# Kernel optimization log

Hardware: AMD Instinct MI355X
Metric: run time of the kernel (lower is better)

The kernel has to match this reference:

```python
import jax, jax.numpy as jnp
import numpy as np

B, T, C, H = 2048, 64, 128, 8
HD = C // H  # head_size = 16
EPS = 1e-5


def layernorm(x, gamma, beta):
    mean = x.mean(-1, keepdims=True)
    var = ((x - mean) ** 2).mean(-1, keepdims=True)  # unbiased=False
    return gamma * (x - mean) / jnp.sqrt(var + EPS) + beta


def setup_inputs() -> dict:
    key = jax.random.key(0)
    ks = jax.random.split(key, 12)
    s_attn = 1.0 / np.sqrt(C)
    s_ff1 = 1.0 / np.sqrt(C)
    s_ff2 = 1.0 / np.sqrt(4 * C)
    return {
        "x": jax.random.normal(ks[0], (B, T, C), dtype=jnp.float32),
        # per-head q/k/v projections, stored (in,out) layout: [H, C, HD]
        "wq": jax.random.normal(ks[1], (H, C, HD), dtype=jnp.float32) * s_attn,
        "wk": jax.random.normal(ks[2], (H, C, HD), dtype=jnp.float32) * s_attn,
        "wv": jax.random.normal(ks[3], (H, C, HD), dtype=jnp.float32) * s_attn,
        "w_proj": jax.random.normal(ks[4], (C, C), dtype=jnp.float32) * s_attn,
        "b_proj": jnp.zeros((C,), dtype=jnp.float32),
        "w1": jax.random.normal(ks[5], (C, 4 * C), dtype=jnp.float32) * s_ff1,
        "b1": jnp.zeros((4 * C,), dtype=jnp.float32),
        "w2": jax.random.normal(ks[6], (4 * C, C), dtype=jnp.float32) * s_ff2,
        "b2": jnp.zeros((C,), dtype=jnp.float32),
        "g1": jnp.ones((C,), dtype=jnp.float32),
        "beta1": jnp.zeros((C,), dtype=jnp.float32),
        "g2": jnp.ones((C,), dtype=jnp.float32),
        "beta2": jnp.zeros((C,), dtype=jnp.float32),
    }


def reference(x, wq, wk, wv, w_proj, b_proj, w1, b1, w2, b2, g1, beta1, g2, beta2):
    # Dropout layers act as identity (eval mode).
    h = layernorm(x, g1, beta1)
    q = jnp.einsum("btc,hcd->bhtd", h, wq)
    k = jnp.einsum("btc,hcd->bhtd", h, wk)
    v = jnp.einsum("btc,hcd->bhtd", h, wv)
    wei = jnp.einsum("bhtd,bhsd->bhts", q, k) * (HD ** -0.5)
    Tcur = x.shape[1]
    causal = jnp.tril(jnp.ones((Tcur, Tcur), dtype=bool))
    wei = jnp.where(causal, wei, -jnp.inf)
    wei = jax.nn.softmax(wei, axis=-1)
    attn = jnp.einsum("bhts,bhsd->bhtd", wei, v)
    # concat heads in order along feature dim -> [B, T, C]
    attn = attn.transpose(0, 2, 1, 3).reshape(x.shape[0], Tcur, C)
    x = x + attn @ w_proj + b_proj
    h2 = layernorm(x, g2, beta2)
    ff = jax.nn.gelu(h2 @ w1 + b1, approximate=False) @ w2 + b2
    return x + ff
```

## Files before the change

kernel.cpp:

```cpp
#include <hip/hip_runtime.h>
#include <hip/hip_bf16.h>
#include <math.h>

#define CC  128
#define RLD 136
#define VLD 72

typedef __attribute__((ext_vector_type(8))) short bf16x8;
typedef __attribute__((ext_vector_type(4))) float f32x4;

#define MFMA16(a, b, c) __builtin_amdgcn_mfma_f32_16x16x32_bf16((a), (b), (c), 0, 0, 0)

__device__ __forceinline__ unsigned short f2bf(float f) {
    unsigned int u = __float_as_uint(f);
    u += 0x7FFFu + ((u >> 16) & 1u);
    return (unsigned short)(u >> 16);
}
__device__ __forceinline__ float bf2f(unsigned short h) {
    return __uint_as_float(((unsigned int)h) << 16);
}
__device__ __forceinline__ unsigned int f2bf2u(float lo, float hi) {
    __hip_bfloat162 h = __float22bfloat162_rn(make_float2(lo, hi));
    union { __hip_bfloat162 h2; unsigned int u; } cv; cv.h2 = h;
    return cv.u;
}
__device__ __forceinline__ bf16x8 mk_bf16x8(unsigned int a0, unsigned int a1,
                                            unsigned int a2, unsigned int a3) {
    union { uint4 u; bf16x8 b; } cv;
    cv.u = make_uint4(a0, a1, a2, a3);
    return cv.b;
}
__device__ __forceinline__ float gelu_tanh(float v) {
    float t = v * fmaf(0.102951871f, v * v, 2.302110084f);
    float s = __builtin_amdgcn_exp2f(t);
    return v - v * __builtin_amdgcn_rcpf(1.0f + s);
}

__global__ void pack_w(const float* __restrict__ src, unsigned short* __restrict__ dst,
                       int K, int N, int mode, float scale) {
    int i = blockIdx.x * 256 + threadIdx.x;
    if (i >= K * N) return;
    int j   = i & 7;
    int l   = (i >> 3) & 63;
    int tkt = i >> 9;
    int KT  = K >> 5;
    int nt  = tkt / KT;
    int kt  = tkt - nt * KT;
    int lg  = l >> 4;
    int k;
    if (mode == 2) {
        int kp = (j < 4) ? (lg * 4 + j) : (16 + lg * 4 + (j - 4));
        k = kt * 32 + kp;
    } else {
        k = kt * 32 + lg * 8 + j;
    }
    int n = nt * 16 + (l & 15);
    float v = (mode == 1) ? src[(n >> 4) * (K * 16) + k * 16 + (n & 15)]
                          : src[k * N + n];
    dst[i] = f2bf(v * scale);
}

#define OQ  0
#define OKk 16384
#define OV  32768
#define OP  49152
#define O1  65536
#define O2  131072

__global__ __launch_bounds__(512, 4) void block_fused(
    const float* __restrict__ x,
    const unsigned short* __restrict__ wpk,
    const float* __restrict__ bp,
    const float* __restrict__ b1, const float* __restrict__ b2,
    const float* __restrict__ g1, const float* __restrict__ be1,
    const float* __restrict__ g2, const float* __restrict__ be2,
    float* __restrict__ out)
{
    __shared__ __align__(16) unsigned short A [9216];
    __shared__ __align__(16) unsigned short Bq[8704];
    __shared__ __align__(16) unsigned short Ck[8704];
    __shared__ __align__(16) unsigned short Vv[9216];

    const int tid  = threadIdx.x;
    const int lane = tid & 63;
    const int wave = tid >> 6;
    const int l15  = lane & 15;
    const int lg   = lane >> 4;

    const float* xb = x   + (size_t)blockIdx.x * (64 * CC);
    float*       ob = out + (size_t)blockIdx.x * (64 * CC);

    {
        float ga = g1[lane], gb = g1[lane + 64], ba = be1[lane], bb = be1[lane + 64];
        for (int r = wave * 8; r < wave * 8 + 8; ++r) {
            float v0 = xb[r * CC + lane], v1 = xb[r * CC + lane + 64];
            float s = v0 + v1;
            float q = fmaf(v0, v0, v1 * v1);
            #pragma unroll
            for (int off = 32; off; off >>= 1) {
                s += __shfl_xor(s, off);
                q += __shfl_xor(q, off);
            }
            float mean = s * (1.0f / CC);
            float var  = fmaf(-mean, mean, q * (1.0f / CC));
            float rstd = __builtin_amdgcn_rsqf(var + 1e-5f);
            float d0 = v0 - mean, d1 = v1 - mean;
            unsigned int u = f2bf2u(fmaf(ga, d0 * rstd, ba), fmaf(gb, d1 * rstd, bb));
            A[r * RLD + lane]      = (unsigned short)u;
            A[r * RLD + lane + 64] = (unsigned short)(u >> 16);
        }
    }
    __syncthreads();

    const int rt  = wave >> 1;
    const int cg  = wave & 1;
    const int row0 = rt * 16 + lg * 4;
    const int hcol = wave * 16;

    {
        const unsigned short* wqb = wpk + OQ  + wave * 2048;
        const unsigned short* wkb = wpk + OKk + wave * 2048;
        const unsigned short* wvb = wpk + OV  + wave * 2048;
        bf16x8 wq4[4], wk4[4], wv4[4];
        #pragma unroll
        for (int kt = 0; kt < 4; ++kt) {
            wq4[kt] = *(const bf16x8*)&wqb[(kt * 64 + lane) * 8];
            wk4[kt] = *(const bf16x8*)&wkb[(kt * 64 + lane) * 8];
            wv4[kt] = *(const bf16x8*)&wvb[(kt * 64 + lane) * 8];
        }
        #pragma unroll
        for (int rt2 = 0; rt2 < 4; ++rt2) {
            bf16x8 la[4];
            #pragma unroll
            for (int kt = 0; kt < 4; ++kt)
                la[kt] = *(const bf16x8*)&A[(rt2 * 16 + l15) * RLD + kt * 32 + lg * 8];
            f32x4 cq = {0.f,0.f,0.f,0.f}, ck = {0.f,0.f,0.f,0.f}, cv = {0.f,0.f,0.f,0.f};
            #pragma unroll
            for (int kt = 0; kt < 4; ++kt) {
                cq = MFMA16(la[kt], wq4[kt], cq);
                ck = MFMA16(la[kt], wk4[kt], ck);
                cv = MFMA16(la[kt], wv4[kt], cv);
            }
            int rw = rt2 * 16 + lg * 4;
            unsigned int q01 = f2bf2u(cq[0], cq[1]), q23 = f2bf2u(cq[2], cq[3]);
            unsigned int k01 = f2bf2u(ck[0], ck[1]), k23 = f2bf2u(ck[2], ck[3]);
            unsigned int v01 = f2bf2u(cv[0], cv[1]), v23 = f2bf2u(cv[2], cv[3]);
            int o = rw * RLD + hcol + l15;
            Bq[o]           = (unsigned short)q01;
            Bq[o + RLD]     = (unsigned short)(q01 >> 16);
            Bq[o + 2 * RLD] = (unsigned short)q23;
            Bq[o + 3 * RLD] = (unsigned short)(q23 >> 16);
            Ck[o]           = (unsigned short)k01;
            Ck[o + RLD]     = (unsigned short)(k01 >> 16);
            Ck[o + 2 * RLD] = (unsigned short)k23;
            Ck[o + 3 * RLD] = (unsigned short)(k23 >> 16);
            int vslot = (rt2 >> 1) * 32 + lg * 8 + (rt2 & 1) * 4;
            *(uint2*)&Vv[(hcol + l15) * VLD + vslot] = make_uint2(v01, v23);
        }
    }

    float xpre[16];
    #pragma unroll
    for (int ntl = 0; ntl < 4; ++ntl) {
        int col = (cg * 4 + ntl) * 16 + l15;
        #pragma unroll
        for (int r = 0; r < 4; ++r)
            xpre[ntl * 4 + r] = xb[(row0 + r) * CC + col];
    }

    {
        bf16x8 zf = {0, 0, 0, 0, 0, 0, 0, 0};
        bf16x8 kf[4];
        #pragma unroll
        for (int st = 0; st < 4; ++st)
            kf[st] = (lane < 32) ? *(const bf16x8*)&Ck[(st * 16 + l15) * RLD + hcol + lg * 8] : zf;
        bf16x8 bvf[2];
        #pragma unroll
        for (int kt = 0; kt < 2; ++kt)
            bvf[kt] = *(const bf16x8*)&Vv[(hcol + l15) * VLD + kt * 32 + lg * 8];

        f32x4 ocs[4];
        #pragma unroll
        for (int mt = 0; mt < 4; ++mt) {
            bf16x8 qf = zf;
            if (lane < 32)
                qf = *(const bf16x8*)&Bq[(mt * 16 + l15) * RLD + hcol + lg * 8];
            f32x4 sfr[4];
            #pragma unroll
            for (int st = 0; st < 4; ++st) {
                sfr[st] = (f32x4){0.f, 0.f, 0.f, 0.f};
                if (st <= mt) sfr[st] = MFMA16(kf[st], qf, sfr[st]);
            }
            float e[4][4];
            float sum = 0.f;
            #pragma unroll
            for (int st = 0; st < 4; ++st) {
                #pragma unroll
                for (int r = 0; r < 4; ++r) {
                    float ev = 0.f;
                    if (st < mt) ev = __builtin_amdgcn_exp2f(sfr[st][r]);
                    else if (st == mt)
                        ev = (lg * 4 + r <= l15) ? __builtin_amdgcn_exp2f(sfr[st][r]) : 0.f;
                    e[st][r] = ev;
                    sum += ev;
                }
            }
            sum += __shfl_xor(sum, 16);
            sum += __shfl_xor(sum, 32);
            float inv = __builtin_amdgcn_rcpf(sum);
            unsigned int u[4][2];
            #pragma unroll
            for (int st = 0; st < 4; ++st) {
                if (st <= mt) {
                    u[st][0] = f2bf2u(e[st][0] * inv, e[st][1] * inv);
                    u[st][1] = f2bf2u(e[st][2] * inv, e[st][3] * inv);
                } else { u[st][0] = 0u; u[st][1] = 0u; }
            }
            f32x4 oc = {0.f, 0.f, 0.f, 0.f};
            #pragma unroll
            for (int kt = 0; kt < 2; ++kt) {
                if (kt <= (mt >> 1)) {
                    bf16x8 pa = mk_bf16x8(u[2 * kt][0], u[2 * kt][1],
                                          u[2 * kt + 1][0], u[2 * kt + 1][1]);
                    oc = MFMA16(pa, bvf[kt], oc);
                }
            }
            ocs[mt] = oc;
        }
        #pragma unroll
        for (int mt = 0; mt < 4; ++mt) {
            unsigned int u01 = f2bf2u(ocs[mt][0], ocs[mt][1]);
            unsigned int u23 = f2bf2u(ocs[mt][2], ocs[mt][3]);
            int o = (mt * 16 + lg * 4) * RLD + hcol + l15;
            Bq[o]           = (unsigned short)u01;
            Bq[o + RLD]     = (unsigned short)(u01 >> 16);
            Bq[o + 2 * RLD] = (unsigned short)u23;
            Bq[o + 3 * RLD] = (unsigned short)(u23 >> 16);
        }
    }
    __syncthreads();

    {
        bf16x8 pa[4];
        #pragma unroll
        for (int kt = 0; kt < 4; ++kt)
            pa[kt] = *(const bf16x8*)&Bq[(rt * 16 + l15) * RLD + kt * 32 + lg * 8];
        #pragma unroll
        for (int ntl = 0; ntl < 4; ++ntl) {
            int nt = cg * 4 + ntl;
            f32x4 c = {0.f, 0.f, 0.f, 0.f};
            #pragma unroll
            for (int kt = 0; kt < 4; ++kt) {
                bf16x8 b = *(const bf16x8*)&wpk[OP + ((nt * 4 + kt) * 64 + lane) * 8];
                c = MFMA16(pa[kt], b, c);
            }
            int col = nt * 16 + l15;
            float bpv = bp[col];
            unsigned int u01 = f2bf2u(xpre[ntl * 4 + 0] + c[0] + bpv,
                                      xpre[ntl * 4 + 1] + c[1] + bpv);
            unsigned int u23 = f2bf2u(xpre[ntl * 4 + 2] + c[2] + bpv,
                                      xpre[ntl * 4 + 3] + c[3] + bpv);
            int o = row0 * RLD + col;
            Ck[o]           = (unsigned short)u01;
            Ck[o + RLD]     = (unsigned short)(u01 >> 16);
            Ck[o + 2 * RLD] = (unsigned short)u23;
            Ck[o + 3 * RLD] = (unsigned short)(u23 >> 16);
        }
    }
    __syncthreads();

    {
        float ga = g2[lane], gb = g2[lane + 64], ba = be2[lane], bb = be2[lane + 64];
        for (int r = wave * 8; r < wave * 8 + 8; ++r) {
            float v0 = bf2f(Ck[r * RLD + lane]), v1 = bf2f(Ck[r * RLD + lane + 64]);
            float s = v0 + v1;
            float q = fmaf(v0, v0, v1 * v1);
            #pragma unroll
            for (int off = 32; off; off >>= 1) {
                s += __shfl_xor(s, off);
                q += __shfl_xor(q, off);
            }
            float mean = s * (1.0f / CC);
            float var  = fmaf(-mean, mean, q * (1.0f / CC));
            float rstd = __builtin_amdgcn_rsqf(var + 1e-5f);
            float d0 = v0 - mean, d1 = v1 - mean;
            unsigned int u = f2bf2u(fmaf(ga, d0 * rstd, ba), fmaf(gb, d1 * rstd, bb));
            A[r * RLD + lane]      = (unsigned short)u;
            A[r * RLD + lane + 64] = (unsigned short)(u >> 16);
        }
    }
    __syncthreads();

    {
        bf16x8 ha[4];
        #pragma unroll
        for (int kt = 0; kt < 4; ++kt)
            ha[kt] = *(const bf16x8*)&A[(rt * 16 + l15) * RLD + kt * 32 + lg * 8];
        f32x4 facc[8];
        #pragma unroll
        for (int n = 0; n < 8; ++n) facc[n] = (f32x4){0.f, 0.f, 0.f, 0.f};

        #pragma unroll 1
        for (int c = 0; c < 8; ++c) {
            int t0 = cg * 16 + 2 * c;
            f32x4 c0 = {0.f,0.f,0.f,0.f}, c1 = {0.f,0.f,0.f,0.f};
            #pragma unroll
            for (int kt = 0; kt < 4; ++kt) {
                bf16x8 w0 = *(const bf16x8*)&wpk[O1 + ((t0 * 4 + kt) * 64 + lane) * 8];
                bf16x8 w1f = *(const bf16x8*)&wpk[O1 + (((t0 + 1) * 4 + kt) * 64 + lane) * 8];
                c0 = MFMA16(w0,  ha[kt], c0);
                c1 = MFMA16(w1f, ha[kt], c1);
            }
            int fb = t0 * 16 + lg * 4;
            float g0[4], g1v[4];
            #pragma unroll
            for (int r = 0; r < 4; ++r) g0[r]  = gelu_tanh(c0[r] + b1[fb + r]);
            #pragma unroll
            for (int r = 0; r < 4; ++r) g1v[r] = gelu_tanh(c1[r] + b1[fb + 16 + r]);
            bf16x8 pa = mk_bf16x8(f2bf2u(g0[0],  g0[1]),  f2bf2u(g0[2],  g0[3]),
                                  f2bf2u(g1v[0], g1v[1]), f2bf2u(g1v[2], g1v[3]));
            int kc = cg * 8 + c;
            #pragma unroll
            for (int nt = 0; nt < 8; ++nt) {
                bf16x8 b = *(const bf16x8*)&wpk[O2 + ((nt * 16 + kc) * 64 + lane) * 8];
                facc[nt] = MFMA16(pa, b, facc[nt]);
            }
        }

        __syncthreads();
        float* fb0 = (rt < 2) ? (float*)A : (float*)Vv;
        const int fbase = (rt & 1) * 2112;
        if (cg == 0) {
            #pragma unroll
            for (int nt = 0; nt < 8; ++nt)
                #pragma unroll
                for (int r = 0; r < 4; ++r)
                    fb0[fbase + (lg * 4 + r) * 132 + nt * 16 + l15] = facc[nt][r];
        }
        __syncthreads();
        if (cg == 1) {
            #pragma unroll
            for (int nt = 0; nt < 8; ++nt) {
                int col = nt * 16 + l15;
                float b2v = b2[col];
                #pragma unroll
                for (int r = 0; r < 4; ++r) {
                    int row = row0 + r;
                    ob[row * CC + col] = bf2f(Ck[row * RLD + col]) + facc[nt][r]
                                       + fb0[fbase + (lg * 4 + r) * 132 + col] + b2v;
                }
            }
        }
    }
}

extern "C" void kernel_launch(void* const* d_in, const int* in_sizes, int n_in,
                              void* d_out, int out_size, void* d_ws, size_t ws_size,
                              hipStream_t stream) {
    (void)n_in; (void)out_size; (void)ws_size;
    const float* x   = (const float*)d_in[0];
    const float* wq  = (const float*)d_in[1];
    const float* wk  = (const float*)d_in[2];
    const float* wv  = (const float*)d_in[3];
    const float* wp  = (const float*)d_in[4];
    const float* bp  = (const float*)d_in[5];
    const float* w1  = (const float*)d_in[6];
    const float* b1  = (const float*)d_in[7];
    const float* w2  = (const float*)d_in[8];
    const float* b2  = (const float*)d_in[9];
    const float* g1  = (const float*)d_in[10];
    const float* be1 = (const float*)d_in[11];
    const float* g2  = (const float*)d_in[12];
    const float* be2 = (const float*)d_in[13];

    unsigned short* ws16 = (unsigned short*)d_ws;
    pack_w<<<64,  256, 0, stream>>>(wq, ws16 + OQ,  128, 128, 1, 0.3606737602f);
    pack_w<<<64,  256, 0, stream>>>(wk, ws16 + OKk, 128, 128, 1, 1.0f);
    pack_w<<<64,  256, 0, stream>>>(wv, ws16 + OV,  128, 128, 1, 1.0f);
    pack_w<<<64,  256, 0, stream>>>(wp, ws16 + OP,  128, 128, 0, 1.0f);
    pack_w<<<256, 256, 0, stream>>>(w1, ws16 + O1,  128, 512, 0, 1.0f);
    pack_w<<<256, 256, 0, stream>>>(w2, ws16 + O2,  512, 128, 2, 1.0f);

    int nblk = in_sizes[0] / (64 * CC);
    block_fused<<<dim3(nblk), dim3(512), 0, stream>>>(
        x, ws16, bp, b1, b2, g1, be1, g2, be2, (float*)d_out);
}
```

Baseline: 146.3 us.

## Fuse LN2 into proj epilogue and keep fp32 residual in registers

Computes the second layernorm's row statistics directly from the projection MFMA accumulators using shuffle reductions plus a small cross-wave LDS exchange, instead of a separate bf16 LDS round trip and a per-row wave reduction pass. The fp32 residual x2 stays in registers and is reused for the final output, which removes the bf16 rounding of the residual. The final split-K reduction is also balanced so both column groups exchange half their accumulators and each writes half the outputs. This costs 16 extra registers per thread and uses Vv/Ck as scratch buffers.

```diff
diff --git a/kernel.cpp b/kernel.cpp
--- a/kernel.cpp
+++ b/kernel.cpp
@@ -5,6 +5,7 @@
 #define CC  128
 #define RLD 136
 #define VLD 72
+#define XLD 130
 
 typedef __attribute__((ext_vector_type(8))) short bf16x8;
 typedef __attribute__((ext_vector_type(4))) float f32x4;
@@ -240,11 +241,14 @@
     }
     __syncthreads();
 
+    float x2r[16];
+    float mean4[4], rstd4[4];
     {
         bf16x8 pa[4];
         #pragma unroll
         for (int kt = 0; kt < 4; ++kt)
             pa[kt] = *(const bf16x8*)&Bq[(rt * 16 + l15) * RLD + kt * 32 + lg * 8];
+        float s4[4] = {0.f, 0.f, 0.f, 0.f}, q4[4] = {0.f, 0.f, 0.f, 0.f};
         #pragma unroll
         for (int ntl = 0; ntl < 4; ++ntl) {
             int nt = cg * 4 + ntl;
@@ -254,39 +258,61 @@
                 bf16x8 b = *(const bf16x8*)&wpk[OP + ((nt * 4 + kt) * 64 + lane) * 8];
                 c = MFMA16(pa[kt], b, c);
             }
-            int col = nt * 16 + l15;
-            float bpv = bp[col];
-            unsigned int u01 = f2bf2u(xpre[ntl * 4 + 0] + c[0] + bpv,
-                                      xpre[ntl * 4 + 1] + c[1] + bpv);
-            unsigned int u23 = f2bf2u(xpre[ntl * 4 + 2] + c[2] + bpv,
-                                      xpre[ntl * 4 + 3] + c[3] + bpv);
+            float bpv = bp[nt * 16 + l15];
+            #pragma unroll
+            for (int r = 0; r < 4; ++r) {
+                float v = xpre[ntl * 4 + r] + c[r] + bpv;
+                x2r[ntl * 4 + r] = v;
+                s4[r] += v;
+                q4[r] = fmaf(v, v, q4[r]);
+            }
+        }
+        #pragma unroll
+        for (int off = 1; off < 16; off <<= 1) {
+            #pragma unroll
+            for (int r = 0; r < 4; ++r) {
+                s4[r] += __shfl_xor(s4[r], off);
+                q4[r] += __shfl_xor(q4[r], off);
+            }
+        }
+        float* sqf = (float*)Vv;
+        if (l15 == 0) {
+            #pragma unroll
+            for (int r = 0; r < 4; ++r) {
+                int idx = (((rt * 2 + cg) * 16) + lg * 4 + r) * 2;
+                sqf[idx]     = s4[r];
+                sqf[idx + 1] = q4[r];
+            }
+        }
+    }
+    __syncthreads();
+    {
+        const float* sqf = (const float*)Vv;
+        #pragma unroll
+        for (int r = 0; r < 4; ++r) {
+            int row = lg * 4 + r;
+            float st = sqf[(((rt * 2 + 0) * 16) + row) * 2]     + sqf[(((rt * 2 + 1) * 16) + row) * 2];
+            float qt = sqf[(((rt * 2 + 0) * 16) + row) * 2 + 1] + sqf[(((rt * 2 + 1) * 16) + row) * 2 + 1];
+            float mean = st * (1.0f / CC);
+            float var  = fmaf(-mean, mean, qt * (1.0f / CC));
+            mean4[r] = mean;
+            rstd4[r] = __builtin_amdgcn_rsqf(var + 1e-5f);
+        }
+        #pragma unroll
+        for (int ntl = 0; ntl < 4; ++ntl) {
+            int col = (cg * 4 + ntl) * 16 + l15;
+            float g = g2[col], be = be2[col];
+            float h0 = fmaf(g, (x2r[ntl * 4 + 0] - mean4[0]) * rstd4[0], be);
+            float h1 = fmaf(g, (x2r[ntl * 4 + 1] - mean4[1]) * rstd4[1], be);
+            float h2v = fmaf(g, (x2r[ntl * 4 + 2] - mean4[2]) * rstd4[2], be);
+            float h3 = fmaf(g, (x2r[ntl * 4 + 3] - mean4[3]) * rstd4[3], be);
+            unsigned int u01 = f2bf2u(h0, h1);
+            unsigned int u23 = f2bf2u(h2v, h3);
             int o = row0 * RLD + col;
-            Ck[o]           = (unsigned short)u01;
-            Ck[o + RLD]     = (unsigned short)(u01 >> 16);
-            Ck[o + 2 * RLD] = (unsigned short)u23;
-            Ck[o + 3 * RLD] = (unsigned short)(u23 >> 16);
-        }
-    }
-    __syncthreads();
-
-    {
-        float ga = g2[lane], gb = g2[lane + 64], ba = be2[lane], bb = be2[lane + 64];
-        for (int r = wave * 8; r < wave * 8 + 8; ++r) {
-            float v0 = bf2f(Ck[r * RLD + lane]), v1 = bf2f(Ck[r * RLD + lane + 64]);
-            float s = v0 + v1;
-            float q = fmaf(v0, v0, v1 * v1);
-            #pragma unroll
-            for (int off = 32; off; off >>= 1) {
-                s += __shfl_xor(s, off);
-                q += __shfl_xor(q, off);
-            }
-            float mean = s * (1.0f / CC);
-            float var  = fmaf(-mean, mean, q * (1.0f / CC));
-            float rstd = __builtin_amdgcn_rsqf(var + 1e-5f);
-            float d0 = v0 - mean, d1 = v1 - mean;
-            unsigned int u = f2bf2u(fmaf(ga, d0 * rstd, ba), fmaf(gb, d1 * rstd, bb));
-            A[r * RLD + lane]      = (unsigned short)u;
-            A[r * RLD + lane + 64] = (unsigned short)(u >> 16);
+            A[o]           = (unsigned short)u01;
+            A[o + RLD]     = (unsigned short)(u01 >> 16);
+            A[o + 2 * RLD] = (unsigned short)u23;
+            A[o + 3 * RLD] = (unsigned short)(u23 >> 16);
         }
     }
     __syncthreads();
@@ -306,7 +332,7 @@
             f32x4 c0 = {0.f,0.f,0.f,0.f}, c1 = {0.f,0.f,0.f,0.f};
             #pragma unroll
             for (int kt = 0; kt < 4; ++kt) {
-                bf16x8 w0 = *(const bf16x8*)&wpk[O1 + ((t0 * 4 + kt) * 64 + lane) * 8];
+                bf16x8 w0  = *(const bf16x8*)&wpk[O1 + ((t0 * 4 + kt) * 64 + lane) * 8];
                 bf16x8 w1f = *(const bf16x8*)&wpk[O1 + (((t0 + 1) * 4 + kt) * 64 + lane) * 8];
                 c0 = MFMA16(w0,  ha[kt], c0);
                 c1 = MFMA16(w1f, ha[kt], c1);
@@ -328,27 +354,29 @@
         }
 
         __syncthreads();
-        float* fb0 = (rt < 2) ? (float*)A : (float*)Vv;
-        const int fbase = (rt & 1) * 2112;
-        if (cg == 0) {
-            #pragma unroll
-            for (int nt = 0; nt < 8; ++nt)
+        float* exb = (rt < 2) ? (float*)A : (float*)Ck;
+        const int fbase = (rt & 1) * (16 * XLD);
+        {
+            int nts = (cg == 0) ? 4 : 0;
+            #pragma unroll
+            for (int n2 = 0; n2 < 4; ++n2) {
+                int nt = nts + n2;
                 #pragma unroll
                 for (int r = 0; r < 4; ++r)
-                    fb0[fbase + (lg * 4 + r) * 132 + nt * 16 + l15] = facc[nt][r];
+                    exb[fbase + (lg * 4 + r) * XLD + nt * 16 + l15] = facc[nt][r];
+            }
         }
         __syncthreads();
-        if (cg == 1) {
-            #pragma unroll
-            for (int nt = 0; nt < 8; ++nt) {
-                int col = nt * 16 + l15;
-                float b2v = b2[col];
-                #pragma unroll
-                for (int r = 0; r < 4; ++r) {
-                    int row = row0 + r;
-                    ob[row * CC + col] = bf2f(Ck[row * RLD + col]) + facc[nt][r]
-                                       + fb0[fbase + (lg * 4 + r) * 132 + col] + b2v;
-                }
+        #pragma unroll
+        for (int n2 = 0; n2 < 4; ++n2) {
+            int nt = cg * 4 + n2;
+            int col = nt * 16 + l15;
+            float b2v = b2[col];
+            #pragma unroll
+            for (int r = 0; r < 4; ++r) {
+                int row = row0 + r;
+                ob[row * CC + col] = x2r[n2 * 4 + r] + facc[nt][r]
+                                   + exb[fbase + (lg * 4 + r) * XLD + col] + b2v;
             }
         }
     }
```

Measured after the change: 222.6 us. +52.1%, slower.
